# Optimization experiments

Hardware: AMD Instinct MI355X
Metric: run time of the kernel (lower is better)

## Reference

```python
import jax, jax.numpy as jnp
import numpy as np

H = W = 512; CELL = 8; P = 16; GX = GY = 64; NGH = GX // 2
SHIFTS = ((0, 0), (1, 0), (0, 1), (1, 1))
EPS = 1e-8
TWO_PI = 2.0 * np.pi

def _diff_round(x):
    return x - jnp.sin(x * TWO_PI) / TWO_PI

def _harder_diff_round(x):
    return _diff_round(_diff_round(x))

def _patches(pad_arr, sx, sy):
    # pad_arr: (H+2*CELL, W+2*CELL, C) -> (NGH*NGH, P, P, C) overlapping supervoxel patches
    x0 = sx * CELL + CELL - (P - CELL) // 2
    y0 = sy * CELL + CELL - (P - CELL) // 2
    s = pad_arr[x0:x0 + NGH * P, y0:y0 + NGH * P]
    c = s.shape[-1]
    return s.reshape(NGH, P, NGH, P, c).transpose(0, 2, 1, 3, 4).reshape(NGH * NGH, P, P, c)

def _conv_trio(x, w, b):
    y = jax.lax.conv_general_dilated(x, w, (1, 1), 'SAME', dimension_numbers=('NHWC', 'HWIO', 'NHWC'))
    return jax.nn.relu(y + b)

def _mlp(x, w0, b0, w1, b1, w2, b2, w3, b3):
    # mlp_features=[5,5,5] with relu, final linear projection to latent_size=10
    x = jax.nn.relu(x @ w0 + b0)
    x = jax.nn.relu(x @ w1 + b1)
    x = jax.nn.relu(x @ w2 + b2)
    return x @ w3 + b3

def _forward(curr_image, curr_label, masks, conv1_w, conv1_b, conv2_w, conv2_b, dense1_w, dense1_b,
             we0, be0, we1, be1, we2, be2, we3, be3, wn0, bn0, wn1, bn1, wn2, bn2, wn3, bn3,
             wout, bout, senders, receivers):
    ids = jnp.arange(GX * GY, dtype=masks.dtype).reshape(GX, GY)
    img, lab, msk = curr_image[0], curr_label[0], masks[0]
    pad_img = jnp.pad(img, ((CELL, CELL), (CELL, CELL), (0, 0)))
    pad_lab = jnp.pad(lab, ((CELL, CELL), (CELL, CELL), (0, 0)))
    pad_msk = jnp.pad(msk[..., None], ((CELL, CELL), (CELL, CELL), (0, 0)), constant_values=-1.0)
    toks, lsv = [], []
    for sx, sy in SHIFTS:  # fixed 4 shift groups (structural, not data loop)
        cid = ids[sx::2, sy::2].reshape(-1)                                    # (F,)
        filt = (_patches(pad_msk, sx, sy)[..., 0] == cid[:, None, None]).astype(img.dtype)  # (F,P,P)
        toks.append(_patches(pad_img, sx, sy) * filt[..., None])              # masked image patches
        lp = _patches(pad_lab, sx, sy)[..., 0]
        summ = jnp.sum(filt, axis=(1, 2))
        lsv.append(_harder_diff_round(jnp.sum(lp * filt, axis=(1, 2)) / (summ + EPS)))
    tokens = jnp.concatenate(toks, axis=0)      # (N, P, P, 1), N = GX*GY
    label_svs = jnp.concatenate(lsv, axis=0)    # (N,)
    x = _conv_trio(tokens, conv1_w, conv1_b)
    x = _conv_trio(x, conv2_w, conv2_b)
    nodes = jax.nn.relu(x.reshape(x.shape[0], -1) @ dense1_w + dense1_b)      # (N, 6)
    n = nodes.shape[0]; e = senders.shape[0]
    ones_e = jnp.ones((e, 1), nodes.dtype)      # broadcast global context [[1]]
    edge_feat = _mlp(jnp.concatenate([nodes[senders], nodes[receivers], ones_e], -1),
                     we0, be0, we1, be1, we2, be2, we3, be3)                   # (E, 10)
    agg = jax.ops.segment_sum(edge_feat, receivers, num_segments=n)            # (N, 10)
    ones_n = jnp.ones((n, 1), nodes.dtype)
    new_nodes = _mlp(jnp.concatenate([nodes, agg, ones_n], -1),
                     wn0, bn0, wn1, bn1, wn2, bn2, wn3, bn3)                   # (N, 10)
    logits = new_nodes @ wout + bout                                           # (N, 2)
    labels2 = jnp.stack([1.0 - label_svs, label_svs], axis=-1)
    return -jnp.sum(labels2 * jax.nn.log_softmax(logits, axis=-1), axis=-1)    # (N,)

def setup_inputs():
    key = jax.random.key(0)
    ks = jax.random.split(key, 32)
    def w(i, shape):
        fan = int(np.prod(shape[:-1]))
        return jax.random.normal(ks[i], shape, jnp.float32) / np.sqrt(fan)
    curr_image = jax.random.normal(ks[0], (1, H, W, 1), jnp.float32)
    curr_label = (jax.random.uniform(ks[1], (1, H, W, 1)) > 0.5).astype(jnp.float32)
    # masks: per-pixel supervoxel id = id of containing 8x8 grid cell
    ids = np.arange(GX * GY, dtype=np.float32).reshape(GX, GY)
    masks = jnp.asarray(np.repeat(np.repeat(ids, CELL, 0), CELL, 1))[None]  # (1, H, W)
    # node index consistent with group-concatenation order of tokens
    node_id = np.zeros((GX, GY), dtype=np.int32)
    for g, (sx, sy) in enumerate(SHIFTS):
        node_id[sx::2, sy::2] = g * NGH * NGH + np.arange(NGH * NGH, dtype=np.int32).reshape(NGH, NGH)
    a = node_id[:, :-1].ravel(); b = node_id[:, 1:].ravel()
    c = node_id[:-1, :].ravel(); d = node_id[1:, :].ravel()
    senders = jnp.asarray(np.concatenate([a, b, c, d]))     # (16128,)
    receivers = jnp.asarray(np.concatenate([b, a, d, c]))
    return dict(curr_image=curr_image, curr_label=curr_label, masks=masks,
                conv1_w=w(2, (3, 3, 1, 40)), conv1_b=jnp.zeros((40,), jnp.float32),
                conv2_w=w(3, (3, 3, 40, 40)), conv2_b=jnp.zeros((40,), jnp.float32),
                dense1_w=w(4, (P * P * 40, 6)), dense1_b=jnp.zeros((6,), jnp.float32),
                we0=w(5, (13, 5)), be0=jnp.zeros((5,), jnp.float32),
                we1=w(6, (5, 5)), be1=jnp.zeros((5,), jnp.float32),
                we2=w(7, (5, 5)), be2=jnp.zeros((5,), jnp.float32),
                we3=w(8, (5, 10)), be3=jnp.zeros((10,), jnp.float32),
                wn0=w(9, (17, 5)), bn0=jnp.zeros((5,), jnp.float32),
                wn1=w(10, (5, 5)), bn1=jnp.zeros((5,), jnp.float32),
                wn2=w(11, (5, 5)), bn2=jnp.zeros((5,), jnp.float32),
                wn3=w(12, (5, 10)), bn3=jnp.zeros((10,), jnp.float32),
                wout=w(13, (10, 2)), bout=jnp.zeros((2,), jnp.float32),
                senders=senders, receivers=receivers)

def reference(curr_image, curr_label, masks, conv1_w, conv1_b, conv2_w, conv2_b, dense1_w, dense1_b,
              we0, be0, we1, be1, we2, be2, we3, be3, wn0, bn0, wn1, bn1, wn2, bn2, wn3, bn3,
              wout, bout, senders, receivers):
    return _forward(curr_image, curr_label, masks, conv1_w, conv1_b, conv2_w, conv2_b, dense1_w, dense1_b,
                    we0, be0, we1, be1, we2, be2, we3, be3, wn0, bn0, wn1, bn1, wn2, bn2, wn3, bn3,
                    wout, bout, senders, receivers)
```

## Files before the change

kernel.cpp:

```cpp
#include <hip/hip_runtime.h>
#include <math.h>


typedef __attribute__((ext_vector_type(8))) short short8;
typedef __attribute__((ext_vector_type(4))) float f32x4;

#define ZROW  324
#define NWTB  (12 * 4 * 48 * 8)
#define ND1W  (256 * 48 * 8)

static __device__ __forceinline__ unsigned short f2bf(float x) {
    unsigned int u = __float_as_uint(x);
    u += 0x7FFF + ((u >> 16) & 1);
    return (unsigned short)(u >> 16);
}

static __device__ __forceinline__ float diff_round(float x) {
    const float TP = 6.2831853071795864769f;
    return x - sinf(x * TP) / TP;
}

template<int IN, int OUT>
static __device__ __forceinline__ void mlp_layer(const float* in,
                                                 const float* __restrict__ w,
                                                 const float* __restrict__ b,
                                                 float* out, bool do_relu) {
#pragma unroll
    for (int j = 0; j < OUT; ++j) {
        float a = b[j];
#pragma unroll
        for (int i = 0; i < IN; ++i) a = fmaf(in[i], w[i * OUT + j], a);
        out[j] = do_relu ? fmaxf(a, 0.f) : a;
    }
}

__global__ __launch_bounds__(256) void k_prep(const float* __restrict__ w2,
                                              const float* __restrict__ d1w,
                                              unsigned short* __restrict__ wTbG,
                                              unsigned short* __restrict__ d1wb) {
    const int i = blockIdx.x * 256 + threadIdx.x;
    if (i < NWTB) {
        const int j    = i & 7;
        const int co   = (i >> 3) % 48;
        const int qg   = (i >> 3) / 48;
        const int quad = qg & 3;
        const int grp  = qg >> 2;
        float val = 0.f;
        if (grp < 9) {
            if (co < 40) val = w2[(grp * 40 + quad * 8 + j) * 40 + co];
        } else {
            const int tap = (grp - 9) * 4 + quad;
            if (tap < 9 && co < 40) val = w2[(tap * 40 + 32 + j) * 40 + co];
        }
        wTbG[i] = f2bf(val);
    } else if (i < NWTB + ND1W) {
        const int jj = i - NWTB;
        const int k  = jj & 7;
        const int co = (jj >> 3) % 48;
        const int px = (jj >> 3) / 48;
        d1wb[jj] = f2bf((co < 40 && k < 6) ? d1w[(px * 40 + co) * 6 + k] : 0.f);
    }
}

__global__ __launch_bounds__(512, 4) void k_patch(
    const float* __restrict__ img, const float* __restrict__ lab,
    const float* __restrict__ msk,
    const float* __restrict__ w1, const float* __restrict__ b1,
    const unsigned short* __restrict__ wTbG,
    const float* __restrict__ b2,
    const unsigned short* __restrict__ d1wb, const float* __restrict__ d1b,
    float* __restrict__ nodes, float* __restrict__ lsv)
{
    __shared__ __align__(16) unsigned short x1[325 * 40];
    __shared__ __align__(16) unsigned short Bs[NWTB];
    __shared__ float p[256];
    __shared__ float red[4][2];
    __shared__ float wsum[8][6];

    const int n = blockIdx.x;
    const int t = threadIdx.x;
    const int g = n >> 10, cell = n & 1023;
    const int gi = cell >> 5, gj = cell & 31;
    const int sx = g & 1, sy = g >> 1;
    const int gx = sx + 2 * gi, gy = sy + 2 * gj;
    const int px0 = gx * 8 - 4, py0 = gy * 8 - 4;
    const float cid = (float)(gx * 64 + gy);

    const int ph = t >> 8, pix = t & 255;
    const int u = pix >> 4, v = pix & 15;
    const int lane = t & 63, wv = t >> 6;
    const int lane15 = t & 15, quad = (t >> 4) & 3;

    float m = -1.f, iv = 0.f, lv = 0.f;
    if (ph == 0) {
        const int r = px0 + u, c = py0 + v;
        if (r >= 0 && r < 512 && c >= 0 && c < 512) {
            m  = msk[r * 512 + c];
            iv = img[r * 512 + c];
            lv = lab[r * 512 + c];
        }
    }

    {
        const uint4* src = (const uint4*)wTbG;
        uint4* dst = (uint4*)Bs;
        for (int i = t; i < NWTB / 8; i += 512) dst[i] = src[i];
    }

    {
        unsigned int* x1w = (unsigned int*)x1;
        for (int i = t; i < 69 * 20; i += 512) {
            const int cellI = i / 20, d = i - cellI * 20;
            int cr;
            if      (cellI < 18) cr = cellI;
            else if (cellI < 36) cr = cellI + 288;
            else if (cellI < 52) cr = (cellI - 35) * 18;
            else if (cellI < 68) cr = (cellI - 51) * 18 + 17;
            else                 cr = ZROW;
            x1w[cr * 20 + d] = 0u;
        }
    }

    const float f = (m == cid) ? 1.f : 0.f;
    if (ph == 0) {
        p[pix] = iv * f;
        float sf = f, slf = lv * f;
        for (int off = 32; off; off >>= 1) {
            sf  += __shfl_down(sf,  off);
            slf += __shfl_down(slf, off);
        }
        if (lane == 0) { red[wv][0] = sf; red[wv][1] = slf; }
    }
    __syncthreads();

    if (t == 0) {
        const float SF = red[0][0] + red[1][0] + red[2][0] + red[3][0];
        const float SL = red[0][1] + red[1][1] + red[2][1] + red[3][1];
        lsv[n] = diff_round(diff_round(SL / (SF + 1e-8f)));
    }

    {
        float nbv[9];
#pragma unroll
        for (int ky = 0; ky < 3; ++ky)
#pragma unroll
            for (int kx = 0; kx < 3; ++kx) {
                const int uy = u + ky - 1, vx = v + kx - 1;
                const bool ok = (uy >= 0) && (uy < 16) && (vx >= 0) && (vx < 16);
                nbv[ky * 3 + kx] = ok ? p[uy * 16 + vx] : 0.f;
            }
        float a1[20];
#pragma unroll
        for (int cc = 0; cc < 20; ++cc) a1[cc] = b1[ph * 20 + cc];
#pragma unroll
        for (int k = 0; k < 9; ++k) {
            const float xv = nbv[k];
#pragma unroll
            for (int cc = 0; cc < 20; ++cc)
                a1[cc] = fmaf(xv, w1[k * 40 + ph * 20 + cc], a1[cc]);
        }
        const int row = (u + 1) * 18 + (v + 1);
        unsigned int* x1w = (unsigned int*)x1;
#pragma unroll
        for (int cg = 0; cg < 10; ++cg) {
            const unsigned int lo = f2bf(fmaxf(a1[2 * cg], 0.f));
            const unsigned int hi = f2bf(fmaxf(a1[2 * cg + 1], 0.f));
            x1w[row * 20 + ph * 10 + cg] = lo | (hi << 16);
        }
    }
    __syncthreads();

    float bias[3];
#pragma unroll
    for (int nt = 0; nt < 3; ++nt) {
        const int co = nt * 16 + lane15;
        bias[nt] = (co < 40) ? b2[co] : 0.f;
    }
    f32x4 acc[2][3];
#pragma unroll
    for (int mt = 0; mt < 2; ++mt)
#pragma unroll
        for (int nt = 0; nt < 3; ++nt) {
            acc[mt][nt][0] = bias[nt]; acc[mt][nt][1] = bias[nt];
            acc[mt][nt][2] = bias[nt]; acc[mt][nt][3] = bias[nt];
        }

#pragma unroll
    for (int tap = 0; tap < 9; ++tap) {
        const int ky = tap / 3, kx = tap % 3;
        short8 bf[3];
#pragma unroll
        for (int nt = 0; nt < 3; ++nt)
            bf[nt] = *(const short8*)(Bs + ((tap * 4 + quad) * 48 + nt * 16 + lane15) * 8);
#pragma unroll
        for (int mt = 0; mt < 2; ++mt) {
            const int arow = (wv * 2 + mt + ky) * 18 + (lane15 + kx);
            const short8 a0 = *(const short8*)(x1 + arow * 40 + quad * 8);
#pragma unroll
            for (int nt = 0; nt < 3; ++nt)
                acc[mt][nt] = __builtin_amdgcn_mfma_f32_16x16x32_bf16(
                    a0, bf[nt], acc[mt][nt], 0, 0, 0);
        }
    }
#pragma unroll
    for (int s = 0; s < 3; ++s) {
        short8 bt[3];
#pragma unroll
        for (int nt = 0; nt < 3; ++nt)
            bt[nt] = *(const short8*)(Bs + (((9 + s) * 4 + quad) * 48 + nt * 16 + lane15) * 8);
        const int tapq = s * 4 + quad;
        const int kyq  = (tapq * 11) >> 5;
        const int kxq  = tapq - 3 * kyq;
#pragma unroll
        for (int mt = 0; mt < 2; ++mt) {
            const int arowq = (wv * 2 + mt + kyq) * 18 + (lane15 + kxq);
            const int offs  = (tapq < 9) ? (arowq * 40 + 32) : (ZROW * 40);
            const short8 at = *(const short8*)(x1 + offs);
#pragma unroll
            for (int nt = 0; nt < 3; ++nt)
                acc[mt][nt] = __builtin_amdgcn_mfma_f32_16x16x32_bf16(
                    at, bt[nt], acc[mt][nt], 0, 0, 0);
        }
    }

    float a6[6] = {0.f, 0.f, 0.f, 0.f, 0.f, 0.f};
#pragma unroll
    for (int mt = 0; mt < 2; ++mt)
#pragma unroll
        for (int nt = 0; nt < 3; ++nt) {
            const int co = nt * 16 + lane15;
#pragma unroll
            for (int reg = 0; reg < 4; ++reg) {
                const int pixel = (wv * 2 + mt) * 16 + quad * 4 + reg;
                const uint4 wq = *(const uint4*)(d1wb + ((pixel * 48 + co) << 3));
                const float a = fmaxf(acc[mt][nt][reg], 0.f);
                a6[0] = fmaf(a, __uint_as_float(wq.x << 16),          a6[0]);
                a6[1] = fmaf(a, __uint_as_float(wq.x & 0xFFFF0000u),  a6[1]);
                a6[2] = fmaf(a, __uint_as_float(wq.y << 16),          a6[2]);
                a6[3] = fmaf(a, __uint_as_float(wq.y & 0xFFFF0000u),  a6[3]);
                a6[4] = fmaf(a, __uint_as_float(wq.z << 16),          a6[4]);
                a6[5] = fmaf(a, __uint_as_float(wq.z & 0xFFFF0000u),  a6[5]);
            }
        }
    for (int off = 32; off; off >>= 1) {
#pragma unroll
        for (int k = 0; k < 6; ++k) a6[k] += __shfl_down(a6[k], off);
    }
    if (lane == 0) {
#pragma unroll
        for (int k = 0; k < 6; ++k) wsum[wv][k] = a6[k];
    }
    __syncthreads();
    if (t < 6) {
        float s = d1b[t];
#pragma unroll
        for (int w = 0; w < 8; ++w) s += wsum[w][t];
        nodes[n * 6 + t] = fmaxf(s, 0.f);
    }
}

__global__ __launch_bounds__(64) void k_node(
    const float* __restrict__ nodes, const float* __restrict__ lsv,
    const float* __restrict__ we0, const float* __restrict__ be0,
    const float* __restrict__ we1, const float* __restrict__ be1,
    const float* __restrict__ we2, const float* __restrict__ be2,
    const float* __restrict__ we3, const float* __restrict__ be3,
    const float* __restrict__ wn0, const float* __restrict__ bn0,
    const float* __restrict__ wn1, const float* __restrict__ bn1,
    const float* __restrict__ wn2, const float* __restrict__ bn2,
    const float* __restrict__ wn3, const float* __restrict__ bn3,
    const float* __restrict__ wout, const float* __restrict__ bout,
    float* __restrict__ out, int N)
{
    const int n = blockIdx.x * 64 + threadIdx.x;
    if (n >= N) return;
    const int g = n >> 10, cell = n & 1023;
    const int gi = cell >> 5, gj = cell & 31;
    const int gx = (g & 1) + 2 * gi, gy = (g >> 1) + 2 * gj;

    float self6[6];
#pragma unroll
    for (int i = 0; i < 6; ++i) self6[i] = nodes[n * 6 + i];

    float agg[10] = {0.f,0.f,0.f,0.f,0.f,0.f,0.f,0.f,0.f,0.f};
    const int DX[4] = {0, 0, -1, 1};
    const int DY[4] = {-1, 1, 0, 0};
#pragma unroll
    for (int d = 0; d < 4; ++d) {
        const int x = gx + DX[d], y = gy + DY[d];
        if (x >= 0 && x < 64 && y >= 0 && y < 64) {
            const int mid = ((x & 1) + 2 * (y & 1)) * 1024 + (x >> 1) * 32 + (y >> 1);
            float in13[13];
#pragma unroll
            for (int i = 0; i < 6; ++i) in13[i] = nodes[mid * 6 + i];
#pragma unroll
            for (int i = 0; i < 6; ++i) in13[6 + i] = self6[i];
            in13[12] = 1.f;
            float h0[5], h1[5], h2[5], o[10];
            mlp_layer<13, 5>(in13, we0, be0, h0, true);
            mlp_layer<5, 5>(h0, we1, be1, h1, true);
            mlp_layer<5, 5>(h1, we2, be2, h2, true);
            mlp_layer<5, 10>(h2, we3, be3, o, false);
#pragma unroll
            for (int j = 0; j < 10; ++j) agg[j] += o[j];
        }
    }

    float in17[17];
#pragma unroll
    for (int i = 0; i < 6; ++i)  in17[i]     = self6[i];
#pragma unroll
    for (int i = 0; i < 10; ++i) in17[6 + i] = agg[i];
    in17[16] = 1.f;
    float h0[5], h1[5], h2[5], o[10];
    mlp_layer<17, 5>(in17, wn0, bn0, h0, true);
    mlp_layer<5, 5>(h0, wn1, bn1, h1, true);
    mlp_layer<5, 5>(h1, wn2, bn2, h2, true);
    mlp_layer<5, 10>(h2, wn3, bn3, o, false);

    float l0 = bout[0], l1 = bout[1];
#pragma unroll
    for (int i = 0; i < 10; ++i) {
        l0 = fmaf(o[i], wout[i * 2 + 0], l0);
        l1 = fmaf(o[i], wout[i * 2 + 1], l1);
    }
    const float mx  = fmaxf(l0, l1);
    const float e0  = expf(l0 - mx), e1 = expf(l1 - mx);
    const float lse = mx + logf(e0 + e1);
    const float sv  = lsv[n];
    out[n] = -((1.f - sv) * (l0 - lse) + sv * (l1 - lse));
}

extern "C" void kernel_launch(void* const* d_in, const int* in_sizes, int n_in,
                              void* d_out, int out_size, void* d_ws, size_t ws_size,
                              hipStream_t stream) {
    (void)n_in; (void)ws_size; (void)in_sizes;
    const float* img = (const float*)d_in[0];
    const float* lab = (const float*)d_in[1];
    const float* msk = (const float*)d_in[2];
    const float* w1  = (const float*)d_in[3];
    const float* b1  = (const float*)d_in[4];
    const float* w2  = (const float*)d_in[5];
    const float* b2  = (const float*)d_in[6];
    const float* d1w = (const float*)d_in[7];
    const float* d1b = (const float*)d_in[8];
    const float* we0 = (const float*)d_in[9],  *be0 = (const float*)d_in[10];
    const float* we1 = (const float*)d_in[11], *be1 = (const float*)d_in[12];
    const float* we2 = (const float*)d_in[13], *be2 = (const float*)d_in[14];
    const float* we3 = (const float*)d_in[15], *be3 = (const float*)d_in[16];
    const float* wn0 = (const float*)d_in[17], *bn0 = (const float*)d_in[18];
    const float* wn1 = (const float*)d_in[19], *bn1 = (const float*)d_in[20];
    const float* wn2 = (const float*)d_in[21], *bn2 = (const float*)d_in[22];
    const float* wn3 = (const float*)d_in[23], *bn3 = (const float*)d_in[24];
    const float* wout = (const float*)d_in[25], *bout = (const float*)d_in[26];
    const int N = out_size;

    char* base = (char*)d_ws;
    float* nodes = (float*)base;
    float* lsvb  = (float*)(base + (size_t)N * 6 * 4);
    unsigned short* wTbG = (unsigned short*)(base + (size_t)N * 7 * 4);
    unsigned short* d1wb = wTbG + NWTB;
    float* out   = (float*)d_out;

    const int prep_n = NWTB + ND1W;
    k_prep<<<(prep_n + 255) / 256, 256, 0, stream>>>(w2, d1w, wTbG, d1wb);
    k_patch<<<N, 512, 0, stream>>>(img, lab, msk, w1, b1, wTbG, b2,
                                   d1wb, d1b, nodes, lsvb);
    k_node<<<(N + 63) / 64, 64, 0, stream>>>(nodes, lsvb,
                                             we0, be0, we1, be1, we2, be2,
                                             we3, be3,
                                             wn0, bn0, wn1, bn1, wn2, bn2,
                                             wn3, bn3, wout, bout, out, N);
}
```

Measured before the change: 216.9 us.

## Shrink LDS footprint to raise occupancy: drop halo rows and stream tail weights

```diff
diff --git a/kernel.cpp b/kernel.cpp
--- a/kernel.cpp
+++ b/kernel.cpp
@@ -5,8 +5,9 @@
 typedef __attribute__((ext_vector_type(8))) short short8;
 typedef __attribute__((ext_vector_type(4))) float f32x4;
 
-#define ZROW  324
+#define ZCELL 288
 #define NWTB  (12 * 4 * 48 * 8)
+#define NMAIN (9 * 4 * 48 * 8)
 #define ND1W  (256 * 48 * 8)
 
 static __device__ __forceinline__ unsigned short f2bf(float x) {
@@ -62,7 +63,7 @@
     }
 }
 
-__global__ __launch_bounds__(512, 4) void k_patch(
+__global__ __launch_bounds__(512, 6) void k_patch(
     const float* __restrict__ img, const float* __restrict__ lab,
     const float* __restrict__ msk,
     const float* __restrict__ w1, const float* __restrict__ b1,
@@ -71,8 +72,8 @@
     const unsigned short* __restrict__ d1wb, const float* __restrict__ d1b,
     float* __restrict__ nodes, float* __restrict__ lsv)
 {
-    __shared__ __align__(16) unsigned short x1[325 * 40];
-    __shared__ __align__(16) unsigned short Bs[NWTB];
+    __shared__ __align__(16) unsigned short x1[289 * 40];
+    __shared__ __align__(16) unsigned short Bs[NMAIN];
     __shared__ float p[256];
     __shared__ float red[4][2];
     __shared__ float wsum[8][6];
@@ -104,19 +105,17 @@
     {
         const uint4* src = (const uint4*)wTbG;
         uint4* dst = (uint4*)Bs;
-        for (int i = t; i < NWTB / 8; i += 512) dst[i] = src[i];
+        for (int i = t; i < NMAIN / 8; i += 512) dst[i] = src[i];
     }
 
     {
         unsigned int* x1w = (unsigned int*)x1;
-        for (int i = t; i < 69 * 20; i += 512) {
-            const int cellI = i / 20, d = i - cellI * 20;
+        for (int i = t; i < 33 * 20; i += 512) {
+            const int cI = i / 20, d = i - cI * 20;
             int cr;
-            if      (cellI < 18) cr = cellI;
-            else if (cellI < 36) cr = cellI + 288;
-            else if (cellI < 52) cr = (cellI - 35) * 18;
-            else if (cellI < 68) cr = (cellI - 51) * 18 + 17;
-            else                 cr = ZROW;
+            if      (cI < 16) cr = cI * 18;
+            else if (cI < 32) cr = (cI - 16) * 18 + 17;
+            else              cr = ZCELL;
             x1w[cr * 20 + d] = 0u;
         }
     }
@@ -159,13 +158,13 @@
             for (int cc = 0; cc < 20; ++cc)
                 a1[cc] = fmaf(xv, w1[k * 40 + ph * 20 + cc], a1[cc]);
         }
-        const int row = (u + 1) * 18 + (v + 1);
+        const int wcell = u * 18 + (v + 1);
         unsigned int* x1w = (unsigned int*)x1;
 #pragma unroll
         for (int cg = 0; cg < 10; ++cg) {
             const unsigned int lo = f2bf(fmaxf(a1[2 * cg], 0.f));
             const unsigned int hi = f2bf(fmaxf(a1[2 * cg + 1], 0.f));
-            x1w[row * 20 + ph * 10 + cg] = lo | (hi << 16);
+            x1w[wcell * 20 + ph * 10 + cg] = lo | (hi << 16);
         }
     }
     __syncthreads();
@@ -185,6 +184,11 @@
             acc[mt][nt][2] = bias[nt]; acc[mt][nt][3] = bias[nt];
         }
 
+    short8 btc[3], btn[3];
+#pragma unroll
+    for (int nt = 0; nt < 3; ++nt)
+        btc[nt] = *(const short8*)(wTbG + ((9 * 4 + quad) * 48 + nt * 16 + lane15) * 8);
+
 #pragma unroll
     for (int tap = 0; tap < 9; ++tap) {
         const int ky = tap / 3, kx = tap % 3;
@@ -194,8 +198,10 @@
             bf[nt] = *(const short8*)(Bs + ((tap * 4 + quad) * 48 + nt * 16 + lane15) * 8);
 #pragma unroll
         for (int mt = 0; mt < 2; ++mt) {
-            const int arow = (wv * 2 + mt + ky) * 18 + (lane15 + kx);
-            const short8 a0 = *(const short8*)(x1 + arow * 40 + quad * 8);
+            const int r = wv * 2 + mt + ky;
+            const int acell = (r == 0 || r == 17) ? ZCELL
+                              : ((r - 1) * 18 + lane15 + kx);
+            const short8 a0 = *(const short8*)(x1 + acell * 40 + quad * 8);
 #pragma unroll
             for (int nt = 0; nt < 3; ++nt)
                 acc[mt][nt] = __builtin_amdgcn_mfma_f32_16x16x32_bf16(
@@ -204,22 +210,29 @@
     }
 #pragma unroll
     for (int s = 0; s < 3; ++s) {
-        short8 bt[3];
-#pragma unroll
-        for (int nt = 0; nt < 3; ++nt)
-            bt[nt] = *(const short8*)(Bs + (((9 + s) * 4 + quad) * 48 + nt * 16 + lane15) * 8);
+        if (s < 2) {
+#pragma unroll
+            for (int nt = 0; nt < 3; ++nt)
+                btn[nt] = *(const short8*)(wTbG +
+                    (((10 + s) * 4 + quad) * 48 + nt * 16 + lane15) * 8);
+        }
         const int tapq = s * 4 + quad;
         const int kyq  = (tapq * 11) >> 5;
         const int kxq  = tapq - 3 * kyq;
 #pragma unroll
         for (int mt = 0; mt < 2; ++mt) {
-            const int arowq = (wv * 2 + mt + kyq) * 18 + (lane15 + kxq);
-            const int offs  = (tapq < 9) ? (arowq * 40 + 32) : (ZROW * 40);
-            const short8 at = *(const short8*)(x1 + offs);
+            const int rq = wv * 2 + mt + kyq;
+            const bool zq = (tapq >= 9) || (rq == 0) || (rq == 17);
+            const int cellq = zq ? ZCELL : ((rq - 1) * 18 + lane15 + kxq);
+            const short8 at = *(const short8*)(x1 + cellq * 40 + 32);
 #pragma unroll
             for (int nt = 0; nt < 3; ++nt)
                 acc[mt][nt] = __builtin_amdgcn_mfma_f32_16x16x32_bf16(
-                    at, bt[nt], acc[mt][nt], 0, 0, 0);
+                    at, btc[nt], acc[mt][nt], 0, 0, 0);
+        }
+        if (s < 2) {
+#pragma unroll
+            for (int nt = 0; nt < 3; ++nt) btc[nt] = btn[nt];
         }
     }
 
```

New measurement: 269.8 us. 1.24x slower.
